# Kernel optimization log

Hardware: AMD Instinct MI355X
Metric: run time of the kernel (lower is better)

Reference implementation:

```python
import jax, jax.numpy as jnp
import numpy as np
from jax import lax

DT = 1.0 / 120.0      # system dt from SystemModel(dt=1/120)
G = 9.81              # gravity for friction force
K_SIGN = 100.0        # smooth sign() sharpness (tanh surrogate, differentiable)
TWO_PI = 2.0 * np.pi


def setup_inputs() -> dict:
    key = jax.random.key(0)
    k1, k2, k3, k4 = jax.random.split(key, 4)
    N, T = 8192, 64
    params = jax.random.uniform(k1, (4,), jnp.float32, 0.05, 0.5)           # friction, damping, tableRes, rimFriction
    covariance_params = jax.random.normal(k2, (7,), jnp.float32) * 0.5 - 5.0  # log-variances
    init_state = jax.random.normal(k3, (N, 6), jnp.float32) * 0.5            # [x, y, vx, vy, theta, omega]
    measurements = jax.random.normal(k4, (N, T, 3), jnp.float32) * 0.5       # [x, y, theta] per step
    return {"params": params, "covariance_params": covariance_params,
            "init_state": init_state, "measurements": measurements}


def reference(params, covariance_params, init_state, measurements):
    """Batched EKF over N segments (vectorized over the Python segment loop of the
    original) with lax.scan over the segment_size timesteps. Returns the mean
    log-likelihood loss: mean over segments of sum_t 0.5*(logdet(S_t) + y_t^T S_t^{-1} y_t),
    with the +-2*pi angle-wrap on the theta innovation as in the original."""
    dyna = jnp.abs(params)
    fric, damp = dyna[0], dyna[1]

    cp = covariance_params
    R = jnp.diag(jnp.exp(cp[:3]))                                            # 3x3 measurement noise
    Q = jnp.diag(jnp.exp(jnp.stack([cp[3], cp[3], cp[4], cp[4], cp[5], cp[6]])))  # 6x6 process noise

    N = init_state.shape[0]
    P0 = jnp.broadcast_to(jnp.eye(6, dtype=init_state.dtype) * 0.01, (N, 6, 6))
    midx = jnp.array([0, 1, 4])
    H = jnp.zeros((3, 6), init_state.dtype).at[0, 0].set(1.).at[1, 1].set(1.).at[2, 4].set(1.)
    I6 = jnp.eye(6, dtype=init_state.dtype)

    def predict(x):
        # free-slide puck dynamics: damping + dry friction (smooth sign)
        pos, vel, th, om = x[:, 0:2], x[:, 2:4], x[:, 4], x[:, 5]
        t = jnp.tanh(K_SIGN * vel)
        pos_n = pos + DT * vel
        vel_n = vel - DT * (damp * vel + fric * G * t)
        th_n = th + DT * om
        om_n = om - DT * damp * om
        return jnp.concatenate([pos_n, vel_n, th_n[:, None], om_n[:, None]], axis=1), t

    def jacobian_F(t):
        # analytic Jacobian of predict; [N,6,6]
        N_ = t.shape[0]
        dv = 1.0 - DT * (damp + fric * G * K_SIGN * (1.0 - t * t))           # [N,2]
        F = jnp.broadcast_to(I6, (N_, 6, 6))
        F = F.at[:, 0, 2].set(DT).at[:, 1, 3].set(DT).at[:, 4, 5].set(DT)
        F = F.at[:, 2, 2].set(dv[:, 0]).at[:, 3, 3].set(dv[:, 1])
        F = F.at[:, 5, 5].set(1.0 - DT * damp)
        return F

    def step(carry, z):
        x, P = carry
        x_pred, t = predict(x)
        F = jacobian_F(t)
        P_pred = jnp.einsum('nij,njk,nlk->nil', F, P, F) + Q                  # F P F^T + Q

        y = z - x_pred[:, midx]                                               # innovation [N,3]
        ang = y[:, 2]
        ang = jnp.where(ang > 1.5 * np.pi, ang - TWO_PI,
                        jnp.where(ang < -1.5 * np.pi, ang + TWO_PI, ang))
        y = y.at[:, 2].set(ang)

        S = P_pred[:, midx, :][:, :, midx] + R                                # [N,3,3]
        Sinv = jnp.linalg.inv(S)
        K = jnp.einsum('nij,njk->nik', P_pred[:, :, midx], Sinv)              # [N,6,3]

        x_new = x_pred + jnp.einsum('nij,nj->ni', K, y)
        KH = jnp.einsum('nij,jk->nik', K, H)                                  # [N,6,6]
        P_new = jnp.einsum('nij,njk->nik', I6 - KH, P_pred)

        _, logdet = jnp.linalg.slogdet(S)
        maha = jnp.einsum('ni,nij,nj->n', y, Sinv, y)
        loss_t = 0.5 * jnp.sum(logdet + maha)
        return (x_new, P_new), loss_t

    (_, _), losses = lax.scan(step, (init_state, P0),
                              jnp.transpose(measurements, (1, 0, 2)))        # scan over T
    return jnp.sum(losses) / N
```

## Files before the change

### kernel.cpp

```cpp
#include <hip/hip_runtime.h>
#include <math.h>

#define DT_STEP (1.0f / 120.0f)
#define G_ACC 9.81f
#define KS 100.0f

__global__ void zero_out_kernel(float* out) { out[0] = 0.0f; }

template <int FT>
__device__ __forceinline__ float run_filter(
    const float fric, const float damp,
    const float R, const float Qp, const float Qv,
    float s0, float s1,
    const float* __restrict__ zp, int T)
{
    const float fG = fric * G_ACC;
    const float a55 = 1.0f - DT_STEP * damp;
    const float PI15 = 4.7123889803846899f;
    const float TWOPI = 6.2831853071795865f;

    float a = 0.01f, b = 0.0f, c = 0.01f;
    float loss = 0.0f;

    float z_cur = zp[0];
    float z_n1 = (T > 1) ? zp[3] : zp[0];

    for (int t = 0; t < T; t++) {
        const float z = z_cur;
        z_cur = z_n1;
        int tn = t + 2; if (tn > T - 1) tn = T - 1;
        z_n1 = zp[3 * tn];

        float s0p, s1p, dv;
        if constexpr (FT < 2) {
            const float e = __expf(2.0f * KS * s1);
            const float th = 1.0f - 2.0f / (e + 1.0f);
            s0p = s0 + DT_STEP * s1;
            s1p = s1 - DT_STEP * (damp * s1 + fG * th);
            dv = 1.0f - DT_STEP * (damp + fG * KS * (1.0f - th * th));
        } else {
            s0p = s0 + DT_STEP * s1;
            s1p = a55 * s1;
            dv = a55;
        }

        const float M00 = a + DT_STEP * b;
        const float M01 = b + DT_STEP * c;
        const float Pp00 = M00 + DT_STEP * M01 + Qp;
        const float Pp01 = dv * M01;
        const float Pp11 = dv * dv * c + Qv;

        float y = z - s0p;
        if constexpr (FT == 2) {
            if (y > PI15) y -= TWOPI;
            else if (y < -PI15) y += TWOPI;
        }

        const float S = Pp00 + R;
        const float Si = 1.0f / S;
        const float K0 = Pp00 * Si;
        const float K1 = Pp01 * Si;

        s0 = s0p + K0 * y;
        s1 = s1p + K1 * y;

        const float omk = 1.0f - K0;
        a = Pp00 * omk;
        b = Pp01 * omk;
        c = Pp11 - K1 * Pp01;

        loss += __logf(S) + y * y * Si;
    }
    return loss;
}

__global__ __launch_bounds__(64) void ekf_split_kernel(
    const float* __restrict__ params,
    const float* __restrict__ cp,
    const float* __restrict__ init_state,
    const float* __restrict__ meas,
    float* __restrict__ out,
    int N, int T)
{
    const int n = blockIdx.x * 64 + threadIdx.x;
    const int ft = blockIdx.y;
    float local = 0.0f;

    if (n < N) {
        const float fric = fabsf(params[0]);
        const float damp = fabsf(params[1]);
        const float* base = init_state + (size_t)n * 6;
        const float* zbase = meas + (size_t)n * T * 3;

        if (ft == 0) {
            const float R = __expf(cp[0]);
            const float Qp = __expf(cp[3]);
            const float Qv = __expf(cp[4]);
            local = run_filter<0>(fric, damp, R, Qp, Qv, base[0], base[2], zbase + 0, T);
        } else if (ft == 1) {
            const float R = __expf(cp[1]);
            const float Qp = __expf(cp[3]);
            const float Qv = __expf(cp[4]);
            local = run_filter<1>(fric, damp, R, Qp, Qv, base[1], base[3], zbase + 1, T);
        } else {
            const float R = __expf(cp[2]);
            const float Qp = __expf(cp[5]);
            const float Qv = __expf(cp[6]);
            local = run_filter<2>(fric, damp, R, Qp, Qv, base[4], base[5], zbase + 2, T);
        }
    }

#pragma unroll
    for (int off = 32; off > 0; off >>= 1)
        local += __shfl_down(local, off, 64);

    if ((threadIdx.x & 63) == 0) {
        atomicAdd(out, local * 0.5f / (float)N);
    }
}

extern "C" void kernel_launch(void* const* d_in, const int* in_sizes, int n_in,
                              void* d_out, int out_size, void* d_ws, size_t ws_size,
                              hipStream_t stream) {
    const float* params     = (const float*)d_in[0];
    const float* cov_params = (const float*)d_in[1];
    const float* init_state = (const float*)d_in[2];
    const float* meas       = (const float*)d_in[3];
    float* out = (float*)d_out;

    const int N = in_sizes[2] / 6;
    const int T = in_sizes[3] / (N * 3);

    zero_out_kernel<<<1, 1, 0, stream>>>(out);

    dim3 grid(N / 64, 3);
    ekf_split_kernel<<<grid, 64, 0, stream>>>(params, cov_params, init_state, meas, out, N, T);
}
```

Baseline: 81.17 us.

## Stage measurement tiles in LDS with coalesced loads and merge filter waves per block

Each block now handles 64 segments with three waves, one per filter channel. The block cooperatively copies the segments' measurement rows from global memory into padded LDS with coalesced loads, then each thread reads its per-step measurement from LDS. This replaces the strided, uncoalesced per-thread global reads of the old kernel. The zeroing kernel launch is also replaced by hipMemsetAsync. In exchange there is a serial staging phase and a barrier before compute, about 49KB of LDS per block that may limit occupancy, and the register prefetch of future measurements is reduced to a single step.

```diff
diff --git a/kernel.cpp b/kernel.cpp
--- a/kernel.cpp
+++ b/kernel.cpp
@@ -4,8 +4,6 @@
 #define DT_STEP (1.0f / 120.0f)
 #define G_ACC 9.81f
 #define KS 100.0f
-
-__global__ void zero_out_kernel(float* out) { out[0] = 0.0f; }
 
 template <int FT>
 __device__ __forceinline__ float run_filter(
@@ -22,14 +20,11 @@
     float a = 0.01f, b = 0.0f, c = 0.01f;
     float loss = 0.0f;
 
-    float z_cur = zp[0];
-    float z_n1 = (T > 1) ? zp[3] : zp[0];
+    float z = zp[0];
 
     for (int t = 0; t < T; t++) {
-        const float z = z_cur;
-        z_cur = z_n1;
-        int tn = t + 2; if (tn > T - 1) tn = T - 1;
-        z_n1 = zp[3 * tn];
+        int tn = t + 1; if (tn > T - 1) tn = T - 1;
+        const float zn = zp[3 * tn];
 
         float s0p, s1p, dv;
         if constexpr (FT < 2) {
@@ -70,11 +65,12 @@
         c = Pp11 - K1 * Pp01;
 
         loss += __logf(S) + y * y * Si;
+        z = zn;
     }
     return loss;
 }
 
-__global__ __launch_bounds__(64) void ekf_split_kernel(
+__global__ __launch_bounds__(192) void ekf_split_lds(
     const float* __restrict__ params,
     const float* __restrict__ cp,
     const float* __restrict__ init_state,
@@ -82,39 +78,47 @@
     float* __restrict__ out,
     int N, int T)
 {
-    const int n = blockIdx.x * 64 + threadIdx.x;
-    const int ft = blockIdx.y;
-    float local = 0.0f;
+    extern __shared__ float zlds[];
+    const int tid = threadIdx.x;
+    const int wave = tid >> 6;
+    const int lane = tid & 63;
+    const int segBase = blockIdx.x * 64;
+    const int row = 3 * T;
+    const int stride = row + 1;
 
-    if (n < N) {
-        const float fric = fabsf(params[0]);
-        const float damp = fabsf(params[1]);
-        const float* base = init_state + (size_t)n * 6;
-        const float* zbase = meas + (size_t)n * T * 3;
+    const float* gsrc = meas + (size_t)segBase * row;
+    for (int s = 0; s < 64; s++) {
+        for (int j = tid; j < row; j += 192)
+            zlds[s * stride + j] = gsrc[(size_t)s * row + j];
+    }
+    __syncthreads();
 
-        if (ft == 0) {
-            const float R = __expf(cp[0]);
-            const float Qp = __expf(cp[3]);
-            const float Qv = __expf(cp[4]);
-            local = run_filter<0>(fric, damp, R, Qp, Qv, base[0], base[2], zbase + 0, T);
-        } else if (ft == 1) {
-            const float R = __expf(cp[1]);
-            const float Qp = __expf(cp[3]);
-            const float Qv = __expf(cp[4]);
-            local = run_filter<1>(fric, damp, R, Qp, Qv, base[1], base[3], zbase + 1, T);
-        } else {
-            const float R = __expf(cp[2]);
-            const float Qp = __expf(cp[5]);
-            const float Qv = __expf(cp[6]);
-            local = run_filter<2>(fric, damp, R, Qp, Qv, base[4], base[5], zbase + 2, T);
-        }
-    }
+    const float fric = fabsf(params[0]);
+    const float damp = fabsf(params[1]);
+
+    const float R  = __expf(cp[wave]);
+    const float Qp = __expf((wave == 2) ? cp[5] : cp[3]);
+    const float Qv = __expf((wave == 2) ? cp[6] : cp[4]);
+
+    const int seg = segBase + lane;
+    const float* sb = init_state + (size_t)seg * 6;
+    const int s0i = (wave == 2) ? 4 : wave;
+    const int s1i = (wave == 2) ? 5 : wave + 2;
+    const float s0 = sb[s0i];
+    const float s1 = sb[s1i];
+
+    const float* zp = zlds + lane * stride + wave;
+
+    float local;
+    if (wave == 0)      local = run_filter<0>(fric, damp, R, Qp, Qv, s0, s1, zp, T);
+    else if (wave == 1) local = run_filter<1>(fric, damp, R, Qp, Qv, s0, s1, zp, T);
+    else                local = run_filter<2>(fric, damp, R, Qp, Qv, s0, s1, zp, T);
 
 #pragma unroll
     for (int off = 32; off > 0; off >>= 1)
         local += __shfl_down(local, off, 64);
 
-    if ((threadIdx.x & 63) == 0) {
+    if (lane == 0) {
         atomicAdd(out, local * 0.5f / (float)N);
     }
 }
@@ -131,8 +135,9 @@
     const int N = in_sizes[2] / 6;
     const int T = in_sizes[3] / (N * 3);
 
-    zero_out_kernel<<<1, 1, 0, stream>>>(out);
+    hipMemsetAsync(out, 0, sizeof(float), stream);
 
-    dim3 grid(N / 64, 3);
-    ekf_split_kernel<<<grid, 64, 0, stream>>>(params, cov_params, init_state, meas, out, N, T);
+    const int grid = N / 64;
+    const size_t shmem = (size_t)64 * (3 * T + 1) * sizeof(float);
+    ekf_split_lds<<<grid, 192, shmem, stream>>>(params, cov_params, init_state, meas, out, N, T);
 }
```

Result: slower. 97.79 us (+20.5%).
